# Performance work log

Measured on AMD Instinct MI355X. Metric: run time of the kernel, lower is better.

## Reference

```python
import jax, jax.numpy as jnp
import numpy as np

F_DIM = 64; HID = 64; HEADS = 2; DH = 32; NG = 4; EPS = 1e-5; SCALE = 8.0  # sqrt(hid_dim)
B = 4; H = 64; W = 64; S = 8; CIN = 64


def _ln(x, g, b):
    mu = x.mean(-1, keepdims=True)
    var = ((x - mu) ** 2).mean(-1, keepdims=True)
    return (x - mu) * jax.lax.rsqrt(var + EPS) * g + b


def _gn(x, g, b):
    # x: [b, C, H, W]; normalize per group over (C/NG, H, W)
    bb, c, hh, ww = x.shape
    xg = x.reshape(bb, NG, -1)
    mu = xg.mean(-1, keepdims=True)
    var = ((xg - mu) ** 2).mean(-1, keepdims=True)
    xn = ((xg - mu) * jax.lax.rsqrt(var + EPS)).reshape(bb, c, hh, ww)
    return xn * g[None, :, None, None] + b[None, :, None, None]


def _mha(xq, xkv, qw, qb, kw, kb, vw, vb, ow, ob):
    # per-head attention with scaling by sqrt(hid_dim) (as in the source)
    q = xq @ qw + qb
    k = xkv @ kw + kb
    v = xkv @ vw + vb
    bb, l, _ = q.shape
    m = k.shape[1]
    qh = q.reshape(bb, l, HEADS, DH)
    kh = k.reshape(bb, m, HEADS, DH)
    vh = v.reshape(bb, m, HEADS, DH)
    s = jnp.einsum('blhd,bmhd->bhlm', qh, kh) / SCALE
    p = jax.nn.softmax(s, axis=-1)
    z = jnp.einsum('bhlm,bmhd->blhd', p, vh).reshape(bb, l, HID)
    return z @ ow + ob


def setup_inputs() -> dict:
    key = jax.random.key(0)
    ks = jax.random.split(key, 34)
    p = lambda k, shp: (jax.random.normal(k, shp, jnp.float32) * 0.02)
    d = {
        'x': jax.random.normal(ks[0], (B, H, W, F_DIM), jnp.float32),
        'slots': jax.random.normal(ks[1], (B, S, CIN), jnp.float32),
        'conv1_w': p(ks[2], (F_DIM, F_DIM)), 'conv1_b': p(ks[3], (F_DIM,)),
        'conv2_w': p(ks[4], (F_DIM, F_DIM)), 'conv2_b': p(ks[5], (F_DIM,)),
        'gn_g': jnp.ones((F_DIM,), jnp.float32), 'gn_b': jnp.zeros((F_DIM,), jnp.float32),
        'ln2_g': jnp.ones((F_DIM,), jnp.float32), 'ln2_b': jnp.zeros((F_DIM,), jnp.float32),
        'ln3_g': jnp.ones((F_DIM,), jnp.float32), 'ln3_b': jnp.zeros((F_DIM,), jnp.float32),
        'ln4_g': jnp.ones((F_DIM,), jnp.float32), 'ln4_b': jnp.zeros((F_DIM,), jnp.float32),
        'sa_qw': p(ks[6], (F_DIM, HID)), 'sa_qb': p(ks[7], (HID,)),
        'sa_kw': p(ks[8], (F_DIM, HID)), 'sa_kb': p(ks[9], (HID,)),
        'sa_vw': p(ks[10], (F_DIM, HID)), 'sa_vb': p(ks[11], (HID,)),
        'sa_ow': p(ks[12], (HID, F_DIM)), 'sa_ob': p(ks[13], (F_DIM,)),
        'ca_qw': p(ks[14], (F_DIM, HID)), 'ca_qb': p(ks[15], (HID,)),
        'ca_kw': p(ks[16], (CIN, HID)), 'ca_kb': p(ks[17], (HID,)),
        'ca_vw': p(ks[18], (CIN, HID)), 'ca_vb': p(ks[19], (HID,)),
        'ca_ow': p(ks[20], (HID, F_DIM)), 'ca_ob': p(ks[21], (F_DIM,)),
        'ff1_w': p(ks[22], (F_DIM, F_DIM)), 'ff1_b': p(ks[23], (F_DIM,)),
    }
    return d


def reference(x, slots, conv1_w, conv1_b, conv2_w, conv2_b, gn_g, gn_b,
              ln2_g, ln2_b, ln3_g, ln3_b, ln4_g, ln4_b,
              sa_qw, sa_qb, sa_kw, sa_kb, sa_vw, sa_vb, sa_ow, sa_ob,
              ca_qw, ca_qb, ca_kw, ca_kb, ca_vw, ca_vb, ca_ow, ca_ob,
              ff1_w, ff1_b):
    b, h, w, f = x.shape
    xc = jnp.transpose(x, (0, 3, 1, 2))               # [b,f,h,w]
    xc = _gn(xc, gn_g, gn_b)
    xc = jnp.einsum('bchw,oc->bohw', xc, conv1_w) + conv1_b[None, :, None, None]
    # faithful to torch: .contiguous().view(b,-1,f) on channels-first layout
    xs = xc.reshape(b, h * w, f)
    # repeat = 1
    xs = jax.nn.gelu(_ln(_mha(xs, xs, sa_qw, sa_qb, sa_kw, sa_kb, sa_vw, sa_vb, sa_ow, sa_ob), ln2_g, ln2_b) + xs, approximate=False)
    xs = _ln(_mha(xs, slots, ca_qw, ca_qb, ca_kw, ca_kb, ca_vw, ca_vb, ca_ow, ca_ob), ln3_g, ln3_b) + xs
    xs = _ln(xs @ ff1_w + ff1_b, ln4_g, ln4_b) + xs
    xo = jnp.transpose(xs.reshape(b, h, w, f), (0, 3, 1, 2))
    xo = jnp.einsum('bchw,oc->bohw', xo, conv2_w) + conv2_b[None, :, None, None]
    return jnp.transpose(xo, (0, 2, 3, 1))
```

## Files before the change

kernel.cpp:

```cpp
#include <hip/hip_runtime.h>
#include <hip/hip_bf16.h>
#include <math.h>

#define NBATCH 4
#define LTOK   4096
#define FD     64

typedef __attribute__((ext_vector_type(8))) short short8v;
typedef __attribute__((ext_vector_type(4))) float f32x4;

static __device__ inline uint32_t packbf2(float a, float b) {
    float2 f; f.x = a; f.y = b;
    __hip_bfloat162 h = __float22bfloat162_rn(f);
    uint32_t u; __builtin_memcpy(&u, &h, 4);
    return u;
}
static __device__ inline ushort packbf1(float a) {
    __hip_bfloat16 h = __float2bfloat16(a);
    ushort u; __builtin_memcpy(&u, &h, 2);
    return u;
}
static __device__ inline float gelu_exact(float y) {
    return 0.5f * y * (1.0f + erff(y * 0.70710678118654752f));
}

__global__ void gn_part_kernel(const float* __restrict__ x,
                               float* __restrict__ partS, float* __restrict__ partSS) {
    const int b = blockIdx.x >> 6, c = blockIdx.x & 63;
    const int t = threadIdx.x, l = t & 63, wv = t >> 6;
    const float4* xb = (const float4*)(x + (size_t)b * 262144) + (size_t)c * 1024;
    float s = 0.f, ss = 0.f;
#pragma unroll
    for (int k = 0; k < 4; k++) {
        float4 v = xb[t + 256 * k];
        s += (v.x + v.y) + (v.z + v.w);
        ss += (v.x * v.x + v.y * v.y) + (v.z * v.z + v.w * v.w);
    }
#pragma unroll
    for (int o = 0; o < 4; o++) {
        const int off = (int[]){1, 2, 16, 32}[o];
        s += __shfl_xor(s, off, 64);
        ss += __shfl_xor(ss, off, 64);
    }
    __shared__ float ls_s[4][4], ls_ss[4][4];
    if ((l & 51) == 0) { ls_s[wv][(l >> 2) & 3] = s; ls_ss[wv][(l >> 2) & 3] = ss; }
    __syncthreads();
    if (t < 4) {
        float S = 0.f, SS = 0.f;
#pragma unroll
        for (int w2 = 0; w2 < 4; w2++) { S += ls_s[w2][t]; SS += ls_ss[w2][t]; }
        partS[b * 256 + t * 64 + c] = S;
        partSS[b * 256 + t * 64 + c] = SS;
    }
}

__global__ void gn_conv1_kernel(const float* __restrict__ x,
                                const float* __restrict__ partS, const float* __restrict__ partSS,
                                const float* __restrict__ gg, const float* __restrict__ gb,
                                const float* __restrict__ w, const float* __restrict__ bias,
                                float* __restrict__ out) {
    const int b = blockIdx.x >> 6, i = blockIdx.x & 63;
    const int t = threadIdx.x;
    __shared__ float xn[64][65];
    __shared__ float wsm[64][64];
    __shared__ float sm[4], sr[4];
    {
        float sv = partS[b * 256 + t];
        float ssv = partSS[b * 256 + t];
        for (int o = 32; o; o >>= 1) { sv += __shfl_xor(sv, o, 64); ssv += __shfl_xor(ssv, o, 64); }
        if ((t & 63) == 0) {
            float mean = sv * (1.f / 65536.f);
            float var = ssv * (1.f / 65536.f) - mean * mean;
            sm[t >> 6] = mean;
            sr[t >> 6] = rsqrtf(var + 1e-5f);
        }
    }
    __syncthreads();
    {
        const int j = t >> 2, c0 = (t & 3) * 16, g = c0 >> 4;
        const float mean = sm[g], rstd = sr[g];
        const float* src = x + (((size_t)b * 64 + i) * 64 + j) * 64 + c0;
#pragma unroll
        for (int k = 0; k < 4; k++) {
            float4 v = *(const float4*)(src + 4 * k);
            xn[j][c0 + 4 * k + 0] = (v.x - mean) * rstd * gg[c0 + 4 * k + 0] + gb[c0 + 4 * k + 0];
            xn[j][c0 + 4 * k + 1] = (v.y - mean) * rstd * gg[c0 + 4 * k + 1] + gb[c0 + 4 * k + 1];
            xn[j][c0 + 4 * k + 2] = (v.z - mean) * rstd * gg[c0 + 4 * k + 2] + gb[c0 + 4 * k + 2];
            xn[j][c0 + 4 * k + 3] = (v.w - mean) * rstd * gg[c0 + 4 * k + 3] + gb[c0 + 4 * k + 3];
        }
        const int o = t >> 2, cc0 = (t & 3) * 16;
#pragma unroll
        for (int k = 0; k < 16; k++) wsm[cc0 + k][o] = w[o * 64 + cc0 + k];
    }
    __syncthreads();
    const int jj = t & 63, olo = (t >> 6) * 16;
    float acc[16];
#pragma unroll
    for (int oi = 0; oi < 16; oi++) acc[oi] = bias[olo + oi];
    for (int c = 0; c < 64; c++) {
        float xv = xn[jj][c];
#pragma unroll
        for (int oi = 0; oi < 16; oi++) acc[oi] += xv * wsm[c][olo + oi];
    }
#pragma unroll
    for (int oi = 0; oi < 16; oi++)
        out[((size_t)b * LTOK + (size_t)(olo + oi) * 64 + i) * 64 + jj] = acc[oi];
}

__global__ void qkv_kernel(const float* __restrict__ in,
                           const float* __restrict__ qw, const float* __restrict__ qb,
                           const float* __restrict__ kw, const float* __restrict__ kb,
                           const float* __restrict__ vw, const float* __restrict__ vb,
                           ushort* __restrict__ Qo, ushort* __restrict__ Ko, ushort* __restrict__ VTg) {
    __shared__ float xt[64][68];
    __shared__ float wt[64][64];
    __shared__ ushort vtr[64 * 72];
    const int t = threadIdx.x;
    const int ph = blockIdx.y;
    const size_t tok0 = (size_t)blockIdx.x * 64;
    const int b = blockIdx.x >> 6;
    const int tokb0 = (blockIdx.x & 63) * 64;
    const int r = t >> 2, cq = t & 3, olo = cq * 16;
    const float* W = (ph == 0) ? qw : (ph == 1) ? kw : vw;
    const float* Bb = (ph == 0) ? qb : (ph == 1) ? kb : vb;
    {
        const float4* src = (const float4*)(in + tok0 * 64) + (size_t)t * 4;
        float4* dst = (float4*)&xt[r][olo];
#pragma unroll
        for (int k = 0; k < 4; k++) dst[k] = src[k];
        const float4* ws2 = (const float4*)W + (size_t)t * 4;
        float4* wd = (float4*)wt + (size_t)t * 4;
#pragma unroll
        for (int k = 0; k < 4; k++) wd[k] = ws2[k];
    }
    __syncthreads();
    float acc[16];
#pragma unroll
    for (int k = 0; k < 4; k++) {
        float4 bv = *(const float4*)(Bb + olo + 4 * k);
        acc[4 * k] = bv.x; acc[4 * k + 1] = bv.y; acc[4 * k + 2] = bv.z; acc[4 * k + 3] = bv.w;
    }
    for (int f = 0; f < 64; f++) {
        float xv = xt[r][f];
#pragma unroll
        for (int oi = 0; oi < 16; oi++) acc[oi] += xv * wt[f][olo + oi];
    }
    if (ph < 2) {
        const float sc = (ph == 0) ? 0.180336880111f : 1.0f;
        uint32_t u[8];
#pragma unroll
        for (int i = 0; i < 8; i++) u[i] = packbf2(acc[2 * i] * sc, acc[2 * i + 1] * sc);
        ushort* op = (ph == 0 ? Qo : Ko) + (tok0 + r) * 64 + olo;
        *(uint4*)op = make_uint4(u[0], u[1], u[2], u[3]);
        *(uint4*)(op + 8) = make_uint4(u[4], u[5], u[6], u[7]);
    } else {
#pragma unroll
        for (int oi = 0; oi < 16; oi++) vtr[(olo + oi) * 72 + r] = packbf1(acc[oi]);
        __syncthreads();
        const int o = t >> 2, ch = t & 3;
        uint4 a0 = *(const uint4*)&vtr[o * 72 + ch * 16];
        uint4 a1 = *(const uint4*)&vtr[o * 72 + ch * 16 + 8];
        ushort* op = VTg + (size_t)(b * 64 + o) * 4096 + tokb0 + ch * 16;
        *(uint4*)op = a0;
        *(uint4*)(op + 8) = a1;
    }
}

__global__ __launch_bounds__(256) void flash_mfma(const ushort* __restrict__ Q,
                                                  const ushort* __restrict__ K,
                                                  const ushort* __restrict__ VTg,
                                                  float* __restrict__ Zp0, float* __restrict__ Zp1,
                                                  float* __restrict__ Ls) {
    const int qt = blockIdx.x;
    const int bh = blockIdx.y;
    const int ks = blockIdx.z;
    const int b = bh >> 1, h = bh & 1;
    const int t = threadIdx.x;
    const int w = t >> 6, l = t & 63, lg = l >> 4, lq = l & 15;

    __shared__ ushort Ks[2][2048];
    __shared__ ushort VT[2][2048];
    __shared__ ushort Pl[4096];

    const size_t base = (size_t)b * LTOK * 64 + h * 32;
    const size_t vrow0 = (size_t)(b * 64 + h * 32);

    const short8v qf = *(const short8v*)(Q + base + (size_t)(qt * 64 + w * 16 + lq) * 64 + 8 * lg);

    const int krow = t >> 2, kdg = t & 3;
    const int koff = (((krow << 5) + kdg * 8)) ^ ((krow & 7) << 3);
    const int vrow = t >> 3, vc8 = t & 7;
    const int voff = (((vrow << 6) + vc8 * 8)) ^ ((vrow & 7) << 3);
    const ushort* Kg = K + base + (size_t)(ks * 2048 + krow) * 64 + kdg * 8;
    const ushort* Vg = VTg + (vrow0 + vrow) * 4096 + ks * 2048 + vc8 * 8;

    uint4 kq = *(const uint4*)Kg;
    uint4 vq = *(const uint4*)Vg;
    *(uint4*)&Ks[0][koff] = kq;
    *(uint4*)&VT[0][voff] = vq;

    f32x4 accZ[2];
#pragma unroll
    for (int d = 0; d < 2; d++) accZ[d] = (f32x4){0.f, 0.f, 0.f, 0.f};
    float lacc = 0.0f;
    const f32x4 zero4 = {0.f, 0.f, 0.f, 0.f};
    int cur = 0;
    const int pb = w << 10;

    for (int kt = 0; kt < 32; kt++) {
        __syncthreads();
        if (kt < 31) {
            kq = *(const uint4*)(Kg + (size_t)(kt + 1) * 4096);
            vq = *(const uint4*)(Vg + (size_t)(kt + 1) * 64);
        }
        f32x4 s4[4];
#pragma unroll
        for (int tk = 0; tk < 4; tk++) {
            const int kr = tk * 16 + lq;
            const short8v aK = *(const short8v*)&Ks[cur][(((kr << 5) + lg * 8)) ^ ((lq & 7) << 3)];
            s4[tk] = __builtin_amdgcn_mfma_f32_16x16x32_bf16(aK, qf, zero4, 0, 0, 0);
        }
        uint32_t pw[8];
#pragma unroll
        for (int tk = 0; tk < 4; tk++) {
            float p0 = exp2f(s4[tk][0]);
            float p1 = exp2f(s4[tk][1]);
            float p2 = exp2f(s4[tk][2]);
            float p3 = exp2f(s4[tk][3]);
            lacc += (p0 + p1) + (p2 + p3);
            pw[2 * tk]     = packbf2(p0, p1);
            pw[2 * tk + 1] = packbf2(p2, p3);
        }
#pragma unroll
        for (int tk = 0; tk < 4; tk++) {
            const int idx = (((lq << 6) + tk * 16 + lg * 4)) ^ ((lq & 7) << 3);
            *(uint2*)&Pl[pb + idx] = make_uint2(pw[2 * tk], pw[2 * tk + 1]);
        }
#pragma unroll
        for (int kc = 0; kc < 2; kc++) {
            const int ia = (((lq << 6) + kc * 32 + lg * 8)) ^ ((lq & 7) << 3);
            const short8v aP = *(const short8v*)&Pl[pb + ia];
#pragma unroll
            for (int dt = 0; dt < 2; dt++) {
                const int ib = ((((dt * 16 + lq) << 6) + kc * 32 + lg * 8)) ^ ((lq & 7) << 3);
                const short8v bV = *(const short8v*)&VT[cur][ib];
                accZ[dt] = __builtin_amdgcn_mfma_f32_16x16x32_bf16(aP, bV, accZ[dt], 0, 0, 0);
            }
        }
        if (kt < 31) {
            *(uint4*)&Ks[cur ^ 1][koff] = kq;
            *(uint4*)&VT[cur ^ 1][voff] = vq;
        }
        cur ^= 1;
    }

    float* Zo = ks ? Zp1 : Zp0;
#pragma unroll
    for (int rr = 0; rr < 4; rr++) {
        const int qrow = qt * 64 + w * 16 + lg * 4 + rr;
#pragma unroll
        for (int dt = 0; dt < 2; dt++)
            Zo[base + (size_t)qrow * 64 + dt * 16 + lq] = accZ[dt][rr];
    }
    lacc += __shfl_xor(lacc, 16, 64);
    lacc += __shfl_xor(lacc, 32, 64);
    if (l < 16)
        Ls[ks * 32768 + bh * 4096 + qt * 64 + w * 16 + lq] = lacc;
}

__global__ __launch_bounds__(512) void tail_fused(
    const float* __restrict__ Zp0, const float* __restrict__ Zp1,
    const float* __restrict__ Ls, const float* __restrict__ xs0,
    const float* __restrict__ slots,
    const float* __restrict__ ckw, const float* __restrict__ ckb,
    const float* __restrict__ cvw, const float* __restrict__ cvb,
    const float* __restrict__ ow, const float* __restrict__ ob,
    const float* __restrict__ g2, const float* __restrict__ b2,
    const float* __restrict__ qw, const float* __restrict__ qb,
    const float* __restrict__ cow, const float* __restrict__ cob,
    const float* __restrict__ g3, const float* __restrict__ b3,
    const float* __restrict__ fw, const float* __restrict__ fb,
    const float* __restrict__ g4, const float* __restrict__ b4,
    const float* __restrict__ cw, const float* __restrict__ cb,
    float* __restrict__ out)
{
    const int t = threadIdx.x;
    const size_t tok0 = (size_t)blockIdx.x * 64;
    const int b = blockIdx.x >> 6;
    const int r = t >> 3, c = t & 7, olo = c * 8;
    __shared__ float xt[64][68];
    __shared__ float wt[64][64];
    __shared__ float kcs[512], vcs[512], sls[512];

    float acc[8], res[8];

    auto stage_w = [&](const float* W) {
        ((float4*)wt)[2 * t] = ((const float4*)W)[2 * t];
        ((float4*)wt)[2 * t + 1] = ((const float4*)W)[2 * t + 1];
    };
    auto stage_x_res = [&]() {
        float4* xd = (float4*)&xt[r][olo];
        xd[0] = make_float4(res[0], res[1], res[2], res[3]);
        xd[1] = make_float4(res[4], res[5], res[6], res[7]);
    };
    auto load8 = [&](float* dst, const float* p) {
        float4 u0 = *(const float4*)(p + olo);
        float4 u1 = *(const float4*)(p + olo + 4);
        dst[0] = u0.x; dst[1] = u0.y; dst[2] = u0.z; dst[3] = u0.w;
        dst[4] = u1.x; dst[5] = u1.y; dst[6] = u1.z; dst[7] = u1.w;
    };
    auto mm = [&](const float* bias) {
        load8(acc, bias);
        for (int f = 0; f < 64; f++) {
            float xv = xt[r][f];
#pragma unroll
            for (int oi = 0; oi < 8; oi++) acc[oi] += xv * wt[f][olo + oi];
        }
    };
    auto ln = [&](const float* gv, const float* bv, bool dogelu) {
        float s1 = 0.f, s2 = 0.f;
#pragma unroll
        for (int oi = 0; oi < 8; oi++) { s1 += acc[oi]; s2 += acc[oi] * acc[oi]; }
#pragma unroll
        for (int o = 1; o <= 4; o <<= 1) {
            s1 += __shfl_xor(s1, o, 64);
            s2 += __shfl_xor(s2, o, 64);
        }
        float mean = s1 * (1.f / 64.f);
        float var = s2 * (1.f / 64.f) - mean * mean;
        float rstd = rsqrtf(var + 1e-5f);
        float gl[8], bl[8];
        load8(gl, gv); load8(bl, bv);
#pragma unroll
        for (int oi = 0; oi < 8; oi++) {
            float y = (acc[oi] - mean) * rstd * gl[oi] + bl[oi] + res[oi];
            res[oi] = dogelu ? gelu_exact(y) : y;
        }
    };

    {
        if (t < 128) ((float4*)sls)[t] = ((const float4*)(slots + (size_t)b * 512))[t];
        const float4* z0 = (const float4*)(Zp0 + tok0 * 64);
        const float4* z1 = (const float4*)(Zp1 + tok0 * 64);
        float4 a0 = z0[2 * t], a1 = z0[2 * t + 1];
        float4 c0 = z1[2 * t], c1 = z1[2 * t + 1];
        const int hh = olo >> 5;
        const int bh_ = b * 2 + hh;
        const int tokb = (blockIdx.x & 63) * 64 + r;
        const float lt = Ls[bh_ * 4096 + tokb] + Ls[32768 + bh_ * 4096 + tokb];
        const float inv = 1.0f / lt;
        float4* xd = (float4*)&xt[r][olo];
        xd[0] = make_float4((a0.x + c0.x) * inv, (a0.y + c0.y) * inv,
                            (a0.z + c0.z) * inv, (a0.w + c0.w) * inv);
        xd[1] = make_float4((a1.x + c1.x) * inv, (a1.y + c1.y) * inv,
                            (a1.z + c1.z) * inv, (a1.w + c1.w) * inv);
        stage_w(ow);
        float4 r0 = *(const float4*)(xs0 + (tok0 + r) * 64 + olo);
        float4 r1 = *(const float4*)(xs0 + (tok0 + r) * 64 + olo + 4);
        res[0] = r0.x; res[1] = r0.y; res[2] = r0.z; res[3] = r0.w;
        res[4] = r1.x; res[5] = r1.y; res[6] = r1.z; res[7] = r1.w;
    }
    __syncthreads();
    {
        const int j = t >> 6, o = t & 63;
        float ak = ckb[o], av = cvb[o];
#pragma unroll 8
        for (int c2 = 0; c2 < 64; c2++) {
            float sv = sls[j * 64 + c2];
            ak += sv * ckw[c2 * 64 + o];
            av += sv * cvw[c2 * 64 + o];
        }
        kcs[t] = ak; vcs[t] = av;
    }
    mm(ob);
    ln(g2, b2, true);

    __syncthreads();
    stage_x_res();
    stage_w(qw);
    __syncthreads();
    mm(qb);
    {
        float p[8];
        float mx = -3.0e38f;
#pragma unroll
        for (int j = 0; j < 8; j++) {
            float d = 0.f;
#pragma unroll
            for (int i2 = 0; i2 < 8; i2++) d += acc[i2] * kcs[j * 64 + olo + i2];
            d += __shfl_xor(d, 1, 64);
            d += __shfl_xor(d, 2, 64);
            d *= 0.125f;
            p[j] = d;
            mx = fmaxf(mx, d);
        }
        float es = 0.f;
#pragma unroll
        for (int j = 0; j < 8; j++) { p[j] = __expf(p[j] - mx); es += p[j]; }
        float inv = 1.f / es;
#pragma unroll
        for (int oi = 0; oi < 8; oi++) {
            float z = 0.f;
#pragma unroll
            for (int j = 0; j < 8; j++) z += p[j] * vcs[j * 64 + olo + oi];
            acc[oi] = z * inv;
        }
    }

    __syncthreads();
    {
        float4* xd = (float4*)&xt[r][olo];
        xd[0] = make_float4(acc[0], acc[1], acc[2], acc[3]);
        xd[1] = make_float4(acc[4], acc[5], acc[6], acc[7]);
    }
    stage_w(cow);
    __syncthreads();
    mm(cob);
    ln(g3, b3, false);

    __syncthreads();
    stage_x_res();
    stage_w(fw);
    __syncthreads();
    mm(fb);
    ln(g4, b4, false);

    __syncthreads();
    stage_x_res();
    {
        const int o5 = t >> 3, c5 = (t & 7) * 8;
#pragma unroll
        for (int k = 0; k < 8; k++) wt[c5 + k][o5] = cw[o5 * 64 + c5 + k];
    }
    __syncthreads();
    mm(cb);
    float* op = out + (tok0 + r) * 64 + olo;
    *(float4*)op = make_float4(acc[0], acc[1], acc[2], acc[3]);
    *(float4*)(op + 4) = make_float4(acc[4], acc[5], acc[6], acc[7]);
}

extern "C" void kernel_launch(void* const* d_in, const int* in_sizes, int n_in,
                              void* d_out, int out_size, void* d_ws, size_t ws_size,
                              hipStream_t stream) {
    const float* x       = (const float*)d_in[0];
    const float* slots   = (const float*)d_in[1];
    const float* conv1_w = (const float*)d_in[2];
    const float* conv1_b = (const float*)d_in[3];
    const float* conv2_w = (const float*)d_in[4];
    const float* conv2_b = (const float*)d_in[5];
    const float* gn_g    = (const float*)d_in[6];
    const float* gn_b    = (const float*)d_in[7];
    const float* ln2_g   = (const float*)d_in[8];
    const float* ln2_b   = (const float*)d_in[9];
    const float* ln3_g   = (const float*)d_in[10];
    const float* ln3_b   = (const float*)d_in[11];
    const float* ln4_g   = (const float*)d_in[12];
    const float* ln4_b   = (const float*)d_in[13];
    const float* sa_qw   = (const float*)d_in[14];
    const float* sa_qb   = (const float*)d_in[15];
    const float* sa_kw   = (const float*)d_in[16];
    const float* sa_kb   = (const float*)d_in[17];
    const float* sa_vw   = (const float*)d_in[18];
    const float* sa_vb   = (const float*)d_in[19];
    const float* sa_ow   = (const float*)d_in[20];
    const float* sa_ob   = (const float*)d_in[21];
    const float* ca_qw   = (const float*)d_in[22];
    const float* ca_qb   = (const float*)d_in[23];
    const float* ca_kw   = (const float*)d_in[24];
    const float* ca_kb   = (const float*)d_in[25];
    const float* ca_vw   = (const float*)d_in[26];
    const float* ca_vb   = (const float*)d_in[27];
    const float* ca_ow   = (const float*)d_in[28];
    const float* ca_ob   = (const float*)d_in[29];
    const float* ff1_w   = (const float*)d_in[30];
    const float* ff1_b   = (const float*)d_in[31];

    float* ws = (float*)d_ws;
    const size_t NBUF = (size_t)NBATCH * LTOK * FD;
    float* partS  = ws;
    float* partSS = ws + 1024;
    float* A      = ws + 4096;
    ushort* Kb    = (ushort*)(A + NBUF);
    ushort* VTgb  = Kb + NBUF;
    ushort* Qb    = VTgb + NBUF;
    float* Zp1    = (float*)(Qb + NBUF);
    float* Ls     = Zp1 + NBUF;
    float* Zp0    = (float*)d_out;

    gn_part_kernel<<<256, 256, 0, stream>>>(x, partS, partSS);
    gn_conv1_kernel<<<256, 256, 0, stream>>>(x, partS, partSS, gn_g, gn_b, conv1_w, conv1_b, A);
    qkv_kernel<<<dim3(256, 3), 256, 0, stream>>>(A, sa_qw, sa_qb, sa_kw, sa_kb, sa_vw, sa_vb, Qb, Kb, VTgb);
    flash_mfma<<<dim3(64, 8, 2), 256, 0, stream>>>(Qb, Kb, VTgb, Zp0, Zp1, Ls);
    tail_fused<<<256, 512, 0, stream>>>(Zp0, Zp1, Ls, A, slots,
                                        ca_kw, ca_kb, ca_vw, ca_vb,
                                        sa_ow, sa_ob, ln2_g, ln2_b,
                                        ca_qw, ca_qb, ca_ow, ca_ob, ln3_g, ln3_b,
                                        ff1_w, ff1_b, ln4_g, ln4_b,
                                        conv2_w, conv2_b, (float*)d_out);
}
```

Measured before the change: 107.8 us.

## Split flash attention keys four ways and unroll double-buffer loop

```diff
diff --git a/kernel.cpp b/kernel.cpp
--- a/kernel.cpp
+++ b/kernel.cpp
@@ -5,6 +5,7 @@
 #define NBATCH 4
 #define LTOK   4096
 #define FD     64
+#define NIT    16
 
 typedef __attribute__((ext_vector_type(8))) short short8v;
 typedef __attribute__((ext_vector_type(4))) float f32x4;
@@ -170,6 +171,7 @@
                                                   const ushort* __restrict__ K,
                                                   const ushort* __restrict__ VTg,
                                                   float* __restrict__ Zp0, float* __restrict__ Zp1,
+                                                  float* __restrict__ Zp2, float* __restrict__ Zp3,
                                                   float* __restrict__ Ls) {
     const int qt = blockIdx.x;
     const int bh = blockIdx.y;
@@ -178,8 +180,8 @@
     const int t = threadIdx.x;
     const int w = t >> 6, l = t & 63, lg = l >> 4, lq = l & 15;
 
-    __shared__ ushort Ks[2][2048];
-    __shared__ ushort VT[2][2048];
+    __shared__ ushort KsB[2][2048];
+    __shared__ ushort VTB[2][2048];
     __shared__ ushort Pl[4096];
 
     const size_t base = (size_t)b * LTOK * 64 + h * 32;
@@ -188,73 +190,76 @@
     const short8v qf = *(const short8v*)(Q + base + (size_t)(qt * 64 + w * 16 + lq) * 64 + 8 * lg);
 
     const int krow = t >> 2, kdg = t & 3;
-    const int koff = (((krow << 5) + kdg * 8)) ^ ((krow & 7) << 3);
+    const int koff = ((krow << 5) + kdg * 8) ^ ((krow & 7) << 3);
     const int vrow = t >> 3, vc8 = t & 7;
-    const int voff = (((vrow << 6) + vc8 * 8)) ^ ((vrow & 7) << 3);
-    const ushort* Kg = K + base + (size_t)(ks * 2048 + krow) * 64 + kdg * 8;
-    const ushort* Vg = VTg + (vrow0 + vrow) * 4096 + ks * 2048 + vc8 * 8;
-
-    uint4 kq = *(const uint4*)Kg;
-    uint4 vq = *(const uint4*)Vg;
-    *(uint4*)&Ks[0][koff] = kq;
-    *(uint4*)&VT[0][voff] = vq;
+    const int voff = ((vrow << 6) + vc8 * 8) ^ ((vrow & 7) << 3);
+    const ushort* kgp = K + base + (size_t)(ks * NIT * 64 + krow) * 64 + kdg * 8;
+    const ushort* vgp = VTg + (vrow0 + vrow) * 4096 + ks * NIT * 64 + vc8 * 8;
+
+    *(uint4*)&KsB[0][koff] = *(const uint4*)kgp;  kgp += 64 * 64;
+    *(uint4*)&VTB[0][voff] = *(const uint4*)vgp;  vgp += 64;
 
     f32x4 accZ[2];
 #pragma unroll
     for (int d = 0; d < 2; d++) accZ[d] = (f32x4){0.f, 0.f, 0.f, 0.f};
     float lacc = 0.0f;
     const f32x4 zero4 = {0.f, 0.f, 0.f, 0.f};
-    int cur = 0;
     const int pb = w << 10;
 
-    for (int kt = 0; kt < 32; kt++) {
+    auto body = [&](const ushort* Kc, const ushort* Vc, ushort* Kn, ushort* Vn, bool pref) {
         __syncthreads();
-        if (kt < 31) {
-            kq = *(const uint4*)(Kg + (size_t)(kt + 1) * 4096);
-            vq = *(const uint4*)(Vg + (size_t)(kt + 1) * 64);
+        uint4 kq = make_uint4(0, 0, 0, 0), vq = make_uint4(0, 0, 0, 0);
+        if (pref) {
+            kq = *(const uint4*)kgp; kgp += 64 * 64;
+            vq = *(const uint4*)vgp; vgp += 64;
         }
         f32x4 s4[4];
 #pragma unroll
         for (int tk = 0; tk < 4; tk++) {
             const int kr = tk * 16 + lq;
-            const short8v aK = *(const short8v*)&Ks[cur][(((kr << 5) + lg * 8)) ^ ((lq & 7) << 3)];
+            const short8v aK = *(const short8v*)&Kc[((kr << 5) + lg * 8) ^ ((lq & 7) << 3)];
             s4[tk] = __builtin_amdgcn_mfma_f32_16x16x32_bf16(aK, qf, zero4, 0, 0, 0);
         }
         uint32_t pw[8];
 #pragma unroll
         for (int tk = 0; tk < 4; tk++) {
-            float p0 = exp2f(s4[tk][0]);
-            float p1 = exp2f(s4[tk][1]);
-            float p2 = exp2f(s4[tk][2]);
-            float p3 = exp2f(s4[tk][3]);
+            float p0 = __builtin_amdgcn_exp2f(s4[tk][0]);
+            float p1 = __builtin_amdgcn_exp2f(s4[tk][1]);
+            float p2 = __builtin_amdgcn_exp2f(s4[tk][2]);
+            float p3 = __builtin_amdgcn_exp2f(s4[tk][3]);
             lacc += (p0 + p1) + (p2 + p3);
             pw[2 * tk]     = packbf2(p0, p1);
             pw[2 * tk + 1] = packbf2(p2, p3);
         }
 #pragma unroll
         for (int tk = 0; tk < 4; tk++) {
-            const int idx = (((lq << 6) + tk * 16 + lg * 4)) ^ ((lq & 7) << 3);
+            const int idx = ((lq << 6) + tk * 16 + lg * 4) ^ ((lq & 7) << 3);
             *(uint2*)&Pl[pb + idx] = make_uint2(pw[2 * tk], pw[2 * tk + 1]);
         }
 #pragma unroll
         for (int kc = 0; kc < 2; kc++) {
-            const int ia = (((lq << 6) + kc * 32 + lg * 8)) ^ ((lq & 7) << 3);
+            const int ia = ((lq << 6) + kc * 32 + lg * 8) ^ ((lq & 7) << 3);
             const short8v aP = *(const short8v*)&Pl[pb + ia];
 #pragma unroll
             for (int dt = 0; dt < 2; dt++) {
-                const int ib = ((((dt * 16 + lq) << 6) + kc * 32 + lg * 8)) ^ ((lq & 7) << 3);
-                const short8v bV = *(const short8v*)&VT[cur][ib];
+                const int ib = (((dt * 16 + lq) << 6) + kc * 32 + lg * 8) ^ ((lq & 7) << 3);
+                const short8v bV = *(const short8v*)&Vc[ib];
                 accZ[dt] = __builtin_amdgcn_mfma_f32_16x16x32_bf16(aP, bV, accZ[dt], 0, 0, 0);
             }
         }
-        if (kt < 31) {
-            *(uint4*)&Ks[cur ^ 1][koff] = kq;
-            *(uint4*)&VT[cur ^ 1][voff] = vq;
-        }
-        cur ^= 1;
-    }
-
-    float* Zo = ks ? Zp1 : Zp0;
+        if (pref) {
+            *(uint4*)&Kn[koff] = kq;
+            *(uint4*)&Vn[voff] = vq;
+        }
+    };
+
+#pragma unroll 1
+    for (int it = 0; it < NIT / 2; it++) {
+        body(KsB[0], VTB[0], KsB[1], VTB[1], true);
+        body(KsB[1], VTB[1], KsB[0], VTB[0], it < NIT / 2 - 1);
+    }
+
+    float* Zo = (ks == 0) ? Zp0 : (ks == 1) ? Zp1 : (ks == 2) ? Zp2 : Zp3;
 #pragma unroll
     for (int rr = 0; rr < 4; rr++) {
         const int qrow = qt * 64 + w * 16 + lg * 4 + rr;
@@ -270,6 +275,7 @@
 
 __global__ __launch_bounds__(512) void tail_fused(
     const float* __restrict__ Zp0, const float* __restrict__ Zp1,
+    const float* __restrict__ Zp2, const float* __restrict__ Zp3,
     const float* __restrict__ Ls, const float* __restrict__ xs0,
     const float* __restrict__ slots,
     const float* __restrict__ ckw, const float* __restrict__ ckb,
@@ -342,18 +348,27 @@
         if (t < 128) ((float4*)sls)[t] = ((const float4*)(slots + (size_t)b * 512))[t];
         const float4* z0 = (const float4*)(Zp0 + tok0 * 64);
         const float4* z1 = (const float4*)(Zp1 + tok0 * 64);
+        const float4* z2 = (const float4*)(Zp2 + tok0 * 64);
+        const float4* z3 = (const float4*)(Zp3 + tok0 * 64);
         float4 a0 = z0[2 * t], a1 = z0[2 * t + 1];
-        float4 c0 = z1[2 * t], c1 = z1[2 * t + 1];
+        float4 b0 = z1[2 * t], b1 = z1[2 * t + 1];
+        float4 c0 = z2[2 * t], c1 = z2[2 * t + 1];
+        float4 d0 = z3[2 * t], d1 = z3[2 * t + 1];
         const int hh = olo >> 5;
         const int bh_ = b * 2 + hh;
         const int tokb = (blockIdx.x & 63) * 64 + r;
-        const float lt = Ls[bh_ * 4096 + tokb] + Ls[32768 + bh_ * 4096 + tokb];
+        const float lt = Ls[bh_ * 4096 + tokb] + Ls[32768 + bh_ * 4096 + tokb]
+                       + Ls[65536 + bh_ * 4096 + tokb] + Ls[98304 + bh_ * 4096 + tokb];
         const float inv = 1.0f / lt;
         float4* xd = (float4*)&xt[r][olo];
-        xd[0] = make_float4((a0.x + c0.x) * inv, (a0.y + c0.y) * inv,
-                            (a0.z + c0.z) * inv, (a0.w + c0.w) * inv);
-        xd[1] = make_float4((a1.x + c1.x) * inv, (a1.y + c1.y) * inv,
-                            (a1.z + c1.z) * inv, (a1.w + c1.w) * inv);
+        xd[0] = make_float4(((a0.x + b0.x) + (c0.x + d0.x)) * inv,
+                            ((a0.y + b0.y) + (c0.y + d0.y)) * inv,
+                            ((a0.z + b0.z) + (c0.z + d0.z)) * inv,
+                            ((a0.w + b0.w) + (c0.w + d0.w)) * inv);
+        xd[1] = make_float4(((a1.x + b1.x) + (c1.x + d1.x)) * inv,
+                            ((a1.y + b1.y) + (c1.y + d1.y)) * inv,
+                            ((a1.z + b1.z) + (c1.z + d1.z)) * inv,
+                            ((a1.w + b1.w) + (c1.w + d1.w)) * inv);
         stage_w(ow);
         float4 r0 = *(const float4*)(xs0 + (tok0 + r) * 64 + olo);
         float4 r1 = *(const float4*)(xs0 + (tok0 + r) * 64 + olo + 4);
@@ -484,14 +499,16 @@
     ushort* VTgb  = Kb + NBUF;
     ushort* Qb    = VTgb + NBUF;
     float* Zp1    = (float*)(Qb + NBUF);
-    float* Ls     = Zp1 + NBUF;
+    float* Zp2    = Zp1 + NBUF;
+    float* Zp3    = Zp2 + NBUF;
+    float* Ls     = Zp3 + NBUF;
     float* Zp0    = (float*)d_out;
 
     gn_part_kernel<<<256, 256, 0, stream>>>(x, partS, partSS);
     gn_conv1_kernel<<<256, 256, 0, stream>>>(x, partS, partSS, gn_g, gn_b, conv1_w, conv1_b, A);
     qkv_kernel<<<dim3(256, 3), 256, 0, stream>>>(A, sa_qw, sa_qb, sa_kw, sa_kb, sa_vw, sa_vb, Qb, Kb, VTgb);
-    flash_mfma<<<dim3(64, 8, 2), 256, 0, stream>>>(Qb, Kb, VTgb, Zp0, Zp1, Ls);
-    tail_fused<<<256, 512, 0, stream>>>(Zp0, Zp1, Ls, A, slots,
+    flash_mfma<<<dim3(64, 8, 4), 256, 0, stream>>>(Qb, Kb, VTgb, Zp0, Zp1, Zp2, Zp3, Ls);
+    tail_fused<<<256, 512, 0, stream>>>(Zp0, Zp1, Zp2, Zp3, Ls, A, slots,
                                         ca_kw, ca_kb, ca_vw, ca_vb,
                                         sa_ow, sa_ob, ln2_g, ln2_b,
                                         ca_qw, ca_qb, ca_ow, ca_ob, ln3_g, ln3_b,
```

Result: faster. 95.21 us (-11.7%).
